# Performance work log

Measured on AMD Instinct MI355X. Metric: run time of the kernel, lower is better.

## Reference

```python
import jax, jax.numpy as jnp
import numpy as np

K = 512       # knowledge_n = node count AND feature dim
S = 50000     # student_n
E_N = 6       # exer_n (hardcoded as literal 6 in the original forward)
DEG_K = 4     # exercise neighbors per knowledge node
DEG_S = 3     # exercise neighbors per student
NEG_SLOPE = 0.2  # PyG GATConv default


def setup_inputs() -> dict:
    key = jax.random.key(0)
    ks = jax.random.split(key, 10)
    kn_emb = jax.random.normal(ks[0], (K, K), jnp.float32)
    exer_emb = jax.random.normal(ks[1], (E_N, K), jnp.float32)
    all_stu_emb = jax.random.normal(ks[2], (S, K), jnp.float32)
    # k_from_e graph: nodes = [exercises(0..5), knowledge(6..6+K-1)]
    src_ke = jax.random.randint(ks[3], (K * DEG_K,), 0, E_N)
    dst_ke = E_N + jnp.repeat(jnp.arange(K), DEG_K)
    edges_ke = jnp.stack([src_ke, dst_ke]).astype(jnp.int32)   # e -> k
    edges_ek = edges_ke[::-1]                                  # k -> e
    # u_from_e graph: nodes = [exercises(0..5), students(6..6+S-1)]
    src_ue = jax.random.randint(ks[4], (S * DEG_S,), 0, E_N)
    dst_ue = E_N + jnp.repeat(jnp.arange(S), DEG_S)
    edges_ue = jnp.stack([src_ue, dst_ue]).astype(jnp.int32)   # e -> u
    edges_eu = edges_ue[::-1]                                  # u -> e
    sc = 1.0 / np.sqrt(K)
    W_gat = jax.random.normal(ks[5], (4, K, K), jnp.float32) * sc
    a_src = jax.random.normal(ks[6], (4, K), jnp.float32) * sc
    a_dst = jax.random.normal(ks[7], (4, K), jnp.float32) * sc
    b_gat = jnp.zeros((4, K), jnp.float32)
    attn_w = jax.random.normal(ks[8], (3, 2 * K), jnp.float32) / np.sqrt(2 * K)
    attn_b = jnp.zeros((3,), jnp.float32)
    return dict(kn_emb=kn_emb, exer_emb=exer_emb, all_stu_emb=all_stu_emb,
                W_gat=W_gat, a_src=a_src, a_dst=a_dst, b_gat=b_gat,
                attn_w=attn_w, attn_b=attn_b,
                edges_ke=edges_ke, edges_ek=edges_ek,
                edges_ue=edges_ue, edges_eu=edges_eu)


def _gat(x, edges, W, a_s, a_d, b, n):
    """Single-head PyG GATConv with self-loops. edges[0]=src, edges[1]=dst."""
    h = x @ W                                   # [n, K]
    loop = jnp.arange(n, dtype=edges.dtype)
    src = jnp.concatenate([edges[0], loop])
    dst = jnp.concatenate([edges[1], loop])
    alpha_s = h @ a_s                           # [n]
    alpha_d = h @ a_d
    e = jax.nn.leaky_relu(alpha_s[src] + alpha_d[dst], NEG_SLOPE)
    emax = jax.lax.stop_gradient(jax.ops.segment_max(e, dst, num_segments=n))
    ex = jnp.exp(e - emax[dst])
    den = jax.ops.segment_sum(ex, dst, num_segments=n)
    alpha = ex / den[dst]                       # per-dst softmax
    out = jax.ops.segment_sum(alpha[:, None] * h[src], dst, num_segments=n)
    return out + b


def reference(kn_emb, exer_emb, all_stu_emb, W_gat, a_src, a_dst, b_gat,
              attn_w, attn_b, edges_ke, edges_ek, edges_ue, edges_eu):
    e_k = jnp.concatenate([exer_emb, kn_emb], axis=0)        # [6+K, K]
    e_u = jnp.concatenate([exer_emb, all_stu_emb], axis=0)   # [6+S, K]
    n_ek, n_eu = e_k.shape[0], e_u.shape[0]
    k_from_e = _gat(e_k, edges_ke, W_gat[0], a_src[0], a_dst[0], b_gat[0], n_ek)
    e_from_k = _gat(e_k, edges_ek, W_gat[1], a_src[1], a_dst[1], b_gat[1], n_ek)
    u_from_e = _gat(e_u, edges_ue, W_gat[2], a_src[2], a_dst[2], b_gat[2], n_eu)
    e_from_u = _gat(e_u, edges_eu, W_gat[3], a_src[3], a_dst[3], b_gat[3], n_eu)
    # knowledge fusion (softmax over a single column -> all ones, kept faithful)
    D = k_from_e[E_N:]
    s3 = jnp.concatenate([kn_emb, D], axis=1) @ attn_w[0] + attn_b[0]   # [K]
    sc = jax.nn.softmax(s3[:, None], axis=1)
    kn_out = kn_emb + sc[:, 0:1] * D
    # exercise fusion: 2-way attention over knowledge/student messages
    B = e_from_k[:E_N]
    C = e_from_u[:E_N]
    s1 = jnp.concatenate([exer_emb, B], axis=1) @ attn_w[1] + attn_b[1]
    s2 = jnp.concatenate([exer_emb, C], axis=1) @ attn_w[2] + attn_b[2]
    sc2 = jax.nn.softmax(jnp.stack([s1, s2], axis=1), axis=1)           # [6, 2]
    exer_out = exer_emb + sc2[:, 0:1] * B + sc2[:, 1:2] * C
    stu_out = all_stu_emb + u_from_e[E_N:]
    return (kn_out, exer_out, stu_out)
```

## Files before the change

kernel.cpp:

```cpp
#include <hip/hip_runtime.h>

typedef __attribute__((ext_vector_type(4))) float f4;
typedef __attribute__((ext_vector_type(8))) short s8;

__device__ __forceinline__ unsigned short f2bf(float x){
  unsigned u = __float_as_uint(x);
  u += 0x7fffu + ((u >> 16) & 1u);
  return (unsigned short)(u >> 16);
}
__device__ __forceinline__ float lrelu(float v){ return v > 0.f ? v : 0.2f * v; }

__device__ __forceinline__ void gload16(const unsigned short* g, unsigned short* l){
  __builtin_amdgcn_global_load_lds((const __attribute__((address_space(1))) unsigned int*)g,
                                   (__attribute__((address_space(3))) unsigned int*)l, 16, 0, 0);
}

__global__ void prep_pq(const float* __restrict__ Wg, const float* __restrict__ a_src,
                        const float* __restrict__ a_dst, float* __restrict__ pq,
                        float* __restrict__ zbase){
  int tid = blockIdx.x * 256 + threadIdx.x;
  for (int i = tid; i < 18444; i += gridDim.x * 256) zbase[i] = 0.f;
  int wid = tid >> 6, lane = tid & 63;
  for (int task = wid; task < 4096; task += gridDim.x * 4){
    int g = task >> 10, isq = (task >> 9) & 1, r = task & 511;
    const float* w = Wg + ((g * 512 + r) << 9);
    const float* a = (isq ? a_dst : a_src) + g * 512;
    float s = 0.f;
    for (int i = lane; i < 512; i += 64) s += w[i] * a[i];
    for (int off = 32; off; off >>= 1) s += __shfl_down(s, off);
    if (lane == 0) pq[task] = s;
  }
}

__global__ void prep_wt(const float* __restrict__ Wg, unsigned short* __restrict__ W2T,
                        unsigned short* __restrict__ W0T){
  __shared__ float tile[32][33];
  const int b = blockIdx.x;
  const int m = b >> 8;
  const int kb = (b & 15) * 32;
  const int nb = ((b >> 4) & 15) * 32;
  const float* W = Wg + (m == 0 ? 2 * 262144 : 0);
  unsigned short* WT = (m == 0) ? W2T : W0T;
  const int tx = threadIdx.x & 31, ty = threadIdx.x >> 5;
  #pragma unroll
  for (int i = 0; i < 32; i += 8) tile[ty + i][tx] = W[(kb + ty + i) * 512 + nb + tx];
  __syncthreads();
  #pragma unroll
  for (int i = 0; i < 32; i += 8) WT[(nb + ty + i) * 512 + kb + tx] = f2bf(tile[tx][ty + i]);
}

__global__ void prep_scal(const float* __restrict__ exer, const float* __restrict__ pq,
                          float* __restrict__ asE, float* __restrict__ adE){
  const int t = threadIdx.x, wid = t >> 6, lane = t & 63;
  for (int task = wid; task < 48; task += 4){
    int gg = task / 12, rem = task % 12, isq = rem / 6, e = rem % 6;
    const float* X = exer + e * 512;
    const float* V = pq + gg * 1024 + isq * 512;
    float s = 0.f;
    for (int i = lane; i < 512; i += 64) s += X[i] * V[i];
    for (int off = 32; off; off >>= 1) s += __shfl_down(s, off);
    if (lane == 0) (isq ? adE : asE)[gg * 6 + e] = s;
  }
}

__global__ void prep_he(const float* __restrict__ exer, const float* __restrict__ Wg,
                        float* __restrict__ HE2, float* __restrict__ HE0){
  const int b = blockIdx.x;
  const int ks = blockIdx.y;
  const int g = (b < 6) ? 0 : 2;
  const int e = b % 6;
  __shared__ float xs[64];
  const int t = threadIdx.x;
  if (t < 64) xs[t] = exer[e * 512 + ks * 64 + t];
  __syncthreads();
  const float* W = Wg + g * 262144 + ks * 64 * 512;
  float acc = 0.f;
  #pragma unroll 4
  for (int kk = 0; kk < 64; kk++) acc += xs[kk] * W[kk * 512 + t];
  atomicAdd(&((g == 0) ? HE0 : HE2)[e * 512 + t], acc);
}

template<int DEG>
__launch_bounds__(256)
__global__ void pass1(const float* __restrict__ x, const float* __restrict__ pq,
                      int gA, int gB,
                      const float* __restrict__ asE, const float* __restrict__ adE,
                      float* __restrict__ alph, const int* __restrict__ idx,
                      float* __restrict__ Craw, float* __restrict__ den, int M)
{
  __shared__ float sC[3072];
  __shared__ float sDen[6];
  const int tid = threadIdx.x, lane = tid & 63, wid = tid >> 6;
  for (int i = tid; i < 3072; i += 256) sC[i] = 0.f;
  if (tid < 6) sDen[tid] = 0.f;

  const int kb = lane * 8;
  const float* pqA = pq + gA * 1024;
  const float* pqB = pq + gB * 1024;
  f4 pA0 = *(const f4*)(pqA + kb),       pA1 = *(const f4*)(pqA + kb + 4);
  f4 qA0 = *(const f4*)(pqA + 512 + kb), qA1 = *(const f4*)(pqA + 512 + kb + 4);
  f4 pB0 = *(const f4*)(pqB + kb),       pB1 = *(const f4*)(pqB + kb + 4);
  float aseR = asE[gA * 6 + (lane % 6)];
  float adeR = adE[gB * 6 + (lane % 6)];

  float cacc[6][8];
  #pragma unroll
  for (int e = 0; e < 6; e++)
    #pragma unroll
    for (int i = 0; i < 8; i++) cacc[e][i] = 0.f;
  float dacc[6] = {0.f,0.f,0.f,0.f,0.f,0.f};
  __syncthreads();

  const int gw = blockIdx.x * 4 + wid, nw = gridDim.x * 4;
  for (int r = gw; r < M; r += nw){
    const float* xr = x + (size_t)r * 512;
    f4 x0 = *(const f4*)(xr + kb), x1 = *(const f4*)(xr + kb + 4);
    float dP = 0.f, dQ = 0.f, dB = 0.f;
    #pragma unroll
    for (int i = 0; i < 4; i++){
      dP += x0[i]*pA0[i] + x1[i]*pA1[i];
      dQ += x0[i]*qA0[i] + x1[i]*qA1[i];
      dB += x0[i]*pB0[i] + x1[i]*pB1[i];
    }
    #pragma unroll
    for (int off = 1; off < 64; off <<= 1){
      dP += __shfl_xor(dP, off); dQ += __shfl_xor(dQ, off); dB += __shfl_xor(dB, off);
    }
    int ei[DEG];
    #pragma unroll
    for (int j = 0; j < DEG; j++) ei[j] = idx[r * DEG + j];
    float scS = lrelu(dP + dQ);
    float sc[DEG], m = scS;
    #pragma unroll
    for (int j = 0; j < DEG; j++){ sc[j] = lrelu(__shfl(aseR, ei[j]) + dQ); m = fmaxf(m, sc[j]); }
    float eS = __expf(scS - m), sum = eS;
    float ev[DEG];
    #pragma unroll
    for (int j = 0; j < DEG; j++){ ev[j] = __expf(sc[j] - m); sum += ev[j]; }
    float inv = 1.f / sum;
    float val = 0.f;
    if (lane == 0) val = eS * inv;
    else if (lane < 7){
      #pragma unroll
      for (int j = 0; j < DEG; j++) val += (ei[j] == lane - 1) ? ev[j] * inv : 0.f;
    }
    if (lane < 8) alph[(size_t)r * 8 + lane] = val;
    float wj[DEG];
    #pragma unroll
    for (int j = 0; j < DEG; j++) wj[j] = __expf(lrelu(dB + __shfl(adeR, ei[j])));
    #pragma unroll
    for (int e = 0; e < 6; e++){
      float we = 0.f;
      #pragma unroll
      for (int j = 0; j < DEG; j++) we += (ei[j] == e) ? wj[j] : 0.f;
      dacc[e] += we;
      #pragma unroll
      for (int i = 0; i < 4; i++){ cacc[e][i] += we * x0[i]; cacc[e][4+i] += we * x1[i]; }
    }
  }
  #pragma unroll
  for (int e = 0; e < 6; e++)
    #pragma unroll
    for (int i = 0; i < 8; i++)
      atomicAdd(&sC[e * 512 + kb + i], cacc[e][i]);
  if (lane == 0){
    #pragma unroll
    for (int e = 0; e < 6; e++) atomicAdd(&sDen[e], dacc[e]);
  }
  __syncthreads();
  for (int i = tid; i < 3072; i += 256){
    float v = sC[i];
    if (v != 0.f) atomicAdd(&Craw[i], v);
  }
  if (tid < 6) atomicAdd(&den[tid], sDen[tid]);
}

__launch_bounds__(512, 4)
__global__ void gemm_ep(const float* __restrict__ x, const unsigned short* __restrict__ WT,
                        const float* __restrict__ alph, const float* __restrict__ HE,
                        const float* __restrict__ bA, float* __restrict__ outp, int M)
{
  __shared__ __align__(16) unsigned short sB[32768];
  __shared__ __align__(16) float sAl[1024];
  __shared__ __align__(16) float sHEb[384];
  __shared__ __align__(16) float sBias[64];

  const int nwg = gridDim.x;
  const int xcd = blockIdx.x & 7, pos = blockIdx.x >> 3;
  const int wido = xcd * (nwg >> 3) + pos;
  const int mb = wido >> 3, nb = wido & 7;
  const int r0 = mb * 128, n0 = nb * 64;
  const int tid = threadIdx.x, lane = tid & 63, w = tid >> 6;
  const int l16 = lane & 15, lhi = lane >> 4;

  {
    const int row = (tid >> 6), slot = tid & 63;
    #pragma unroll
    for (int it = 0; it < 8; it++){
      const int rr = it * 8 + row;
      const unsigned short* src = WT + (size_t)(n0 + rr) * 512 + ((slot ^ (rr & 7)) << 3);
      gload16(src, sB + it * 4096 + tid * 8);
    }
  }
  if (tid < 256){
    const int row = tid >> 1;
    *(f4*)(sAl + tid * 4) = *(const f4*)(alph + (size_t)min(r0 + row, M - 1) * 8 + (tid & 1) * 4);
  } else if (tid < 352){
    const int idx2 = tid - 256, e = idx2 >> 4, c4 = idx2 & 15;
    *(f4*)(sHEb + e * 64 + c4 * 4) = *(const f4*)(HE + e * 512 + n0 + c4 * 4);
  } else if (tid < 368){
    const int idx2 = tid - 352;
    *(f4*)(sBias + idx2 * 4) = *(const f4*)(bA + n0 + idx2 * 4);
  }
  __syncthreads();

  const int gr0 = r0 + w * 16 + l16;
  const float* xr = x + (size_t)min(gr0, M - 1) * 512 + lhi * 8;

  f4 acc[4];
  #pragma unroll
  for (int n = 0; n < 4; n++) acc[n] = (f4){0.f, 0.f, 0.f, 0.f};

  #pragma unroll 4
  for (int kt = 0; kt < 16; kt++){
    f4 a0 = *(const f4*)(xr + kt * 32);
    f4 a1 = *(const f4*)(xr + kt * 32 + 4);
    s8 af;
    #pragma unroll
    for (int i = 0; i < 4; i++){ af[i] = (short)f2bf(a0[i]); af[4+i] = (short)f2bf(a1[i]); }
    #pragma unroll
    for (int n = 0; n < 4; n++){
      const int row = n * 16 + l16;
      const int slot = ((kt << 2) + lhi) ^ (row & 7);
      s8 bf = *(const s8*)(sB + row * 512 + (slot << 3));
      acc[n] = __builtin_amdgcn_mfma_f32_16x16x32_bf16(af, bf, acc[n], 0, 0, 0);
    }
  }

  float hec[4][6], bias[4];
  #pragma unroll
  for (int n = 0; n < 4; n++){
    bias[n] = sBias[n * 16 + l16];
    #pragma unroll
    for (int e = 0; e < 6; e++) hec[n][e] = sHEb[e * 64 + n * 16 + l16];
  }

  #pragma unroll
  for (int j = 0; j < 4; j++){
    const int rl = w * 16 + lhi * 4 + j;
    const int gr = r0 + rl;
    if (gr < M){
      f4 alA = *(const f4*)(sAl + rl * 8);
      f4 alB = *(const f4*)(sAl + rl * 8 + 4);
      const float aself = alA[0];
      #pragma unroll
      for (int n = 0; n < 4; n++){
        const int gc = n0 + n * 16 + l16;
        float v = x[(size_t)gr * 512 + gc] + aself * acc[n][j] + bias[n];
        v += alA[1] * hec[n][0] + alA[2] * hec[n][1] + alA[3] * hec[n][2];
        v += alB[0] * hec[n][3] + alB[1] * hec[n][4] + alB[2] * hec[n][5];
        outp[(size_t)gr * 512 + gc] = v;
      }
    }
  }
}

__global__ void finalize_bc(const float* __restrict__ exer, const float* __restrict__ Wg,
                            const float* __restrict__ asE, const float* __restrict__ adE,
                            const float* __restrict__ Craw3, const float* __restrict__ den3,
                            const float* __restrict__ Craw1, const float* __restrict__ den1,
                            const float* __restrict__ b_gat, float* __restrict__ B,
                            float* __restrict__ C){
  const int b = blockIdx.x;
  const int ks = blockIdx.y;
  const int isC = (b >= 6) ? 1 : 0;
  const int e = b % 6;
  const int g = isC ? 3 : 1;
  const float* Craw = isC ? Craw3 : Craw1;
  const float* den  = isC ? den3  : den1;
  __shared__ float mix[64];
  const int t = threadIdx.x;
  float aS = asE[g*6 + e], aD = adE[g*6 + e];
  float wself = __expf(lrelu(aS + aD));
  float dn = den[e] + wself;
  if (t < 64){
    int k = ks * 64 + t;
    mix[t] = (Craw[e*512 + k] + wself * exer[e*512 + k]) / dn;
  }
  __syncthreads();
  const float* W = Wg + g * 262144 + ks * 64 * 512;
  float acc = 0.f;
  #pragma unroll 4
  for (int kk = 0; kk < 64; kk++) acc += mix[kk] * W[kk * 512 + t];
  if (ks == 0) acc += b_gat[g*512 + t];
  atomicAdd(&(isC ? C : B)[e*512 + t], acc);
}

__global__ void finalize_exer(const float* __restrict__ exer, const float* __restrict__ B,
                              const float* __restrict__ C, const float* __restrict__ attn_w,
                              const float* __restrict__ attn_b, float* __restrict__ outE){
  __shared__ float s1[6], s2[6];
  const int t = threadIdx.x, wid = t >> 6, lane = t & 63;
  for (int task = wid; task < 12; task += 8){
    int e = task >> 1, which = task & 1;
    const float* w = attn_w + (which + 1) * 1024;
    const float* X = exer + e * 512;
    const float* Y = (which ? C : B) + e * 512;
    float s = 0.f;
    for (int i = lane; i < 512; i += 64) s += X[i] * w[i] + Y[i] * w[512 + i];
    for (int off = 32; off; off >>= 1) s += __shfl_down(s, off);
    if (lane == 0) (which ? s2 : s1)[e] = s + attn_b[which + 1];
  }
  __syncthreads();
  for (int i = t; i < 3072; i += 512){
    int e = i >> 9;
    float a = s1[e], b = s2[e];
    float m = fmaxf(a, b);
    float ea = __expf(a - m), eb = __expf(b - m);
    float inv = 1.f / (ea + eb);
    outE[i] = exer[i] + (ea * inv) * B[i] + (eb * inv) * C[i];
  }
}

extern "C" void kernel_launch(void* const* d_in, const int* in_sizes, int n_in,
                              void* d_out, int out_size, void* d_ws, size_t ws_size,
                              hipStream_t stream){
  const float* kn     = (const float*)d_in[0];
  const float* exer   = (const float*)d_in[1];
  const float* stu    = (const float*)d_in[2];
  const float* Wg     = (const float*)d_in[3];
  const float* a_src  = (const float*)d_in[4];
  const float* a_dst  = (const float*)d_in[5];
  const float* b_gat  = (const float*)d_in[6];
  const float* attn_w = (const float*)d_in[7];
  const float* attn_b = (const float*)d_in[8];
  const int*   e_ke   = (const int*)d_in[9];
  const int*   e_ue   = (const int*)d_in[11];
  float* out = (float*)d_out;

  unsigned short* W2T = (unsigned short*)d_ws;
  unsigned short* W0T = W2T + 262144;
  float* fb    = (float*)(W0T + 262144);
  float* pq    = fb;
  float* asE   = pq + 4096;
  float* adE   = asE + 24;
  float* Craw3 = adE + 24;
  float* Craw1 = Craw3 + 3072;
  float* den3  = Craw1 + 3072;
  float* den1  = den3 + 6;
  float* HE2   = den1 + 6;
  float* HE0   = HE2 + 3072;
  float* Bb    = HE0 + 3072;
  float* Cc    = Bb + 3072;
  float* alphS = Cc + 3072;
  float* alphK = alphS + 400384;

  hipLaunchKernelGGL(prep_pq, dim3(256), dim3(256), 0, stream, Wg, a_src, a_dst, pq, Craw3);
  hipLaunchKernelGGL(prep_wt, dim3(512), dim3(256), 0, stream, Wg, W2T, W0T);
  hipLaunchKernelGGL(prep_scal, dim3(1), dim3(256), 0, stream, exer, pq, asE, adE);
  hipLaunchKernelGGL(prep_he, dim3(12, 8), dim3(512), 0, stream, exer, Wg, HE2, HE0);

  hipLaunchKernelGGL((pass1<3>), dim3(768), dim3(256), 0, stream,
                     stu, pq, 2, 3, asE, adE, alphS, e_ue, Craw3, den3, 50000);
  hipLaunchKernelGGL((pass1<4>), dim3(8), dim3(256), 0, stream,
                     kn, pq, 0, 1, asE, adE, alphK, e_ke, Craw1, den1, 512);

  hipLaunchKernelGGL(gemm_ep, dim3(391 * 8), dim3(512), 0, stream,
                     stu, W2T, alphS, HE2, b_gat + 1024, out + 265216, 50000);
  hipLaunchKernelGGL(gemm_ep, dim3(4 * 8), dim3(512), 0, stream,
                     kn, W0T, alphK, HE0, b_gat, out, 512);

  hipLaunchKernelGGL(finalize_bc, dim3(12, 8), dim3(512), 0, stream,
                     exer, Wg, asE, adE, Craw3, den3, Craw1, den1, b_gat, Bb, Cc);
  hipLaunchKernelGGL(finalize_exer, dim3(1), dim3(512), 0, stream,
                     exer, Bb, Cc, attn_w, attn_b, out + 262144);
}
```

Measured before the change: 485.2 us.

## Fuse attention pass and GEMM epilogue into one kernel with LDS-staged activations

Result: slower. 656.4 us (+35.3%).

```diff
diff --git a/kernel.cpp b/kernel.cpp
--- a/kernel.cpp
+++ b/kernel.cpp
@@ -9,11 +9,6 @@
   return (unsigned short)(u >> 16);
 }
 __device__ __forceinline__ float lrelu(float v){ return v > 0.f ? v : 0.2f * v; }
-
-__device__ __forceinline__ void gload16(const unsigned short* g, unsigned short* l){
-  __builtin_amdgcn_global_load_lds((const __attribute__((address_space(1))) unsigned int*)g,
-                                   (__attribute__((address_space(3))) unsigned int*)l, 16, 0, 0);
-}
 
 __global__ void prep_pq(const float* __restrict__ Wg, const float* __restrict__ a_src,
                         const float* __restrict__ a_dst, float* __restrict__ pq,
@@ -81,186 +76,159 @@
 }
 
 template<int DEG>
-__launch_bounds__(256)
-__global__ void pass1(const float* __restrict__ x, const float* __restrict__ pq,
-                      int gA, int gB,
-                      const float* __restrict__ asE, const float* __restrict__ adE,
-                      float* __restrict__ alph, const int* __restrict__ idx,
-                      float* __restrict__ Craw, float* __restrict__ den, int M)
+__launch_bounds__(512, 4)
+__global__ void fused(const float* __restrict__ x, const unsigned short* __restrict__ WT,
+                      const float* __restrict__ pqA, const float* __restrict__ pqB,
+                      const float* __restrict__ asEg, const float* __restrict__ adEg,
+                      const float* __restrict__ HE, const float* __restrict__ bias,
+                      const int* __restrict__ idx, float* __restrict__ Craw,
+                      float* __restrict__ den, float* __restrict__ outp, int M)
 {
-  __shared__ float sC[3072];
-  __shared__ float sDen[6];
-  const int tid = threadIdx.x, lane = tid & 63, wid = tid >> 6;
-  for (int i = tid; i < 3072; i += 256) sC[i] = 0.f;
-  if (tid < 6) sDen[tid] = 0.f;
-
-  const int kb = lane * 8;
-  const float* pqA = pq + gA * 1024;
-  const float* pqB = pq + gB * 1024;
-  f4 pA0 = *(const f4*)(pqA + kb),       pA1 = *(const f4*)(pqA + kb + 4);
-  f4 qA0 = *(const f4*)(pqA + 512 + kb), qA1 = *(const f4*)(pqA + 512 + kb + 4);
-  f4 pB0 = *(const f4*)(pqB + kb),       pB1 = *(const f4*)(pqB + kb + 4);
-  float aseR = asE[gA * 6 + (lane % 6)];
-  float adeR = adE[gB * 6 + (lane % 6)];
-
-  float cacc[6][8];
-  #pragma unroll
-  for (int e = 0; e < 6; e++)
-    #pragma unroll
-    for (int i = 0; i < 8; i++) cacc[e][i] = 0.f;
-  float dacc[6] = {0.f,0.f,0.f,0.f,0.f,0.f};
-  __syncthreads();
-
-  const int gw = blockIdx.x * 4 + wid, nw = gridDim.x * 4;
-  for (int r = gw; r < M; r += nw){
-    const float* xr = x + (size_t)r * 512;
-    f4 x0 = *(const f4*)(xr + kb), x1 = *(const f4*)(xr + kb + 4);
+  __shared__ __align__(16) unsigned short sA[32768];
+  __shared__ float sMeta[64][16];
+  __shared__ float sDot[3][64];
+
+  const int tid = threadIdx.x, lane = tid & 63, w = tid >> 6;
+  const int r0 = blockIdx.x * 64;
+  const int kseg = (lane ^ w) * 8;
+
+  f4 pP0 = *(const f4*)(pqA + kseg),       pP1 = *(const f4*)(pqA + kseg + 4);
+  f4 pQ0 = *(const f4*)(pqA + 512 + kseg), pQ1 = *(const f4*)(pqA + 512 + kseg + 4);
+  f4 pB0 = *(const f4*)(pqB + kseg),       pB1 = *(const f4*)(pqB + kseg + 4);
+
+  #pragma unroll
+  for (int i = 0; i < 8; i++){
+    const int row = i * 8 + w;
+    const float* xr = x + (size_t)min(r0 + row, M - 1) * 512 + kseg;
+    f4 x0 = *(const f4*)(xr), x1 = *(const f4*)(xr + 4);
     float dP = 0.f, dQ = 0.f, dB = 0.f;
     #pragma unroll
-    for (int i = 0; i < 4; i++){
-      dP += x0[i]*pA0[i] + x1[i]*pA1[i];
-      dQ += x0[i]*qA0[i] + x1[i]*qA1[i];
-      dB += x0[i]*pB0[i] + x1[i]*pB1[i];
+    for (int c = 0; c < 4; c++){
+      dP += x0[c]*pP0[c] + x1[c]*pP1[c];
+      dQ += x0[c]*pQ0[c] + x1[c]*pQ1[c];
+      dB += x0[c]*pB0[c] + x1[c]*pB1[c];
     }
     #pragma unroll
     for (int off = 1; off < 64; off <<= 1){
       dP += __shfl_xor(dP, off); dQ += __shfl_xor(dQ, off); dB += __shfl_xor(dB, off);
     }
+    if (lane == 0){ sDot[0][row] = dP; sDot[1][row] = dQ; sDot[2][row] = dB; }
+    s8 pk;
+    #pragma unroll
+    for (int c = 0; c < 4; c++){ pk[c] = (short)f2bf(x0[c]); pk[4+c] = (short)f2bf(x1[c]); }
+    *(s8*)(sA + row * 512 + lane * 8) = pk;
+  }
+  __syncthreads();
+
+  if (w == 0){
+    const int r = lane, gr = r0 + r;
+    const bool valid = gr < M;
+    const float dP = sDot[0][r], dQ = sDot[1][r], dB = sDot[2][r];
     int ei[DEG];
     #pragma unroll
-    for (int j = 0; j < DEG; j++) ei[j] = idx[r * DEG + j];
+    for (int j = 0; j < DEG; j++) ei[j] = valid ? idx[(size_t)gr * DEG + j] : 0;
     float scS = lrelu(dP + dQ);
     float sc[DEG], m = scS;
     #pragma unroll
-    for (int j = 0; j < DEG; j++){ sc[j] = lrelu(__shfl(aseR, ei[j]) + dQ); m = fmaxf(m, sc[j]); }
+    for (int j = 0; j < DEG; j++){ sc[j] = lrelu(asEg[ei[j]] + dQ); m = fmaxf(m, sc[j]); }
     float eS = __expf(scS - m), sum = eS;
     float ev[DEG];
     #pragma unroll
     for (int j = 0; j < DEG; j++){ ev[j] = __expf(sc[j] - m); sum += ev[j]; }
-    float inv = 1.f / sum;
-    float val = 0.f;
-    if (lane == 0) val = eS * inv;
-    else if (lane < 7){
-      #pragma unroll
-      for (int j = 0; j < DEG; j++) val += (ei[j] == lane - 1) ? ev[j] * inv : 0.f;
-    }
-    if (lane < 8) alph[(size_t)r * 8 + lane] = val;
+    const float inv = 1.f / sum;
+    sMeta[r][0] = valid ? eS * inv : 0.f;
     float wj[DEG];
     #pragma unroll
-    for (int j = 0; j < DEG; j++) wj[j] = __expf(lrelu(dB + __shfl(adeR, ei[j])));
+    for (int j = 0; j < DEG; j++) wj[j] = __expf(lrelu(dB + adEg[ei[j]]));
     #pragma unroll
     for (int e = 0; e < 6; e++){
-      float we = 0.f;
-      #pragma unroll
-      for (int j = 0; j < DEG; j++) we += (ei[j] == e) ? wj[j] : 0.f;
-      dacc[e] += we;
-      #pragma unroll
-      for (int i = 0; i < 4; i++){ cacc[e][i] += we * x0[i]; cacc[e][4+i] += we * x1[i]; }
-    }
-  }
-  #pragma unroll
-  for (int e = 0; e < 6; e++)
-    #pragma unroll
-    for (int i = 0; i < 8; i++)
-      atomicAdd(&sC[e * 512 + kb + i], cacc[e][i]);
-  if (lane == 0){
-    #pragma unroll
-    for (int e = 0; e < 6; e++) atomicAdd(&sDen[e], dacc[e]);
-  }
-  __syncthreads();
-  for (int i = tid; i < 3072; i += 256){
-    float v = sC[i];
-    if (v != 0.f) atomicAdd(&Craw[i], v);
-  }
-  if (tid < 6) atomicAdd(&den[tid], sDen[tid]);
-}
-
-__launch_bounds__(512, 4)
-__global__ void gemm_ep(const float* __restrict__ x, const unsigned short* __restrict__ WT,
-                        const float* __restrict__ alph, const float* __restrict__ HE,
-                        const float* __restrict__ bA, float* __restrict__ outp, int M)
-{
-  __shared__ __align__(16) unsigned short sB[32768];
-  __shared__ __align__(16) float sAl[1024];
-  __shared__ __align__(16) float sHEb[384];
-  __shared__ __align__(16) float sBias[64];
-
-  const int nwg = gridDim.x;
-  const int xcd = blockIdx.x & 7, pos = blockIdx.x >> 3;
-  const int wido = xcd * (nwg >> 3) + pos;
-  const int mb = wido >> 3, nb = wido & 7;
-  const int r0 = mb * 128, n0 = nb * 64;
-  const int tid = threadIdx.x, lane = tid & 63, w = tid >> 6;
+      float ce = 0.f, we = 0.f;
+      #pragma unroll
+      for (int j = 0; j < DEG; j++){
+        ce += (ei[j] == e) ? ev[j] * inv : 0.f;
+        we += (ei[j] == e) ? wj[j] : 0.f;
+      }
+      sMeta[r][1 + e] = valid ? ce : 0.f;
+      we = valid ? we : 0.f;
+      sMeta[r][7 + e] = we;
+      float t = we;
+      #pragma unroll
+      for (int off = 1; off < 64; off <<= 1) t += __shfl_xor(t, off);
+      if (lane == 0) atomicAdd(den + e, t);
+    }
+  }
+
   const int l16 = lane & 15, lhi = lane >> 4;
-
-  {
-    const int row = (tid >> 6), slot = tid & 63;
-    #pragma unroll
-    for (int it = 0; it < 8; it++){
-      const int rr = it * 8 + row;
-      const unsigned short* src = WT + (size_t)(n0 + rr) * 512 + ((slot ^ (rr & 7)) << 3);
-      gload16(src, sB + it * 4096 + tid * 8);
-    }
-  }
-  if (tid < 256){
-    const int row = tid >> 1;
-    *(f4*)(sAl + tid * 4) = *(const f4*)(alph + (size_t)min(r0 + row, M - 1) * 8 + (tid & 1) * 4);
-  } else if (tid < 352){
-    const int idx2 = tid - 256, e = idx2 >> 4, c4 = idx2 & 15;
-    *(f4*)(sHEb + e * 64 + c4 * 4) = *(const f4*)(HE + e * 512 + n0 + c4 * 4);
-  } else if (tid < 368){
-    const int idx2 = tid - 352;
-    *(f4*)(sBias + idx2 * 4) = *(const f4*)(bA + n0 + idx2 * 4);
-  }
-  __syncthreads();
-
-  const int gr0 = r0 + w * 16 + l16;
-  const float* xr = x + (size_t)min(gr0, M - 1) * 512 + lhi * 8;
-
-  f4 acc[4];
-  #pragma unroll
-  for (int n = 0; n < 4; n++) acc[n] = (f4){0.f, 0.f, 0.f, 0.f};
+  const unsigned short* wtb = WT + (size_t)(w * 64 + l16) * 512 + lhi * 8;
+  f4 acc[4][4];
+  #pragma unroll
+  for (int m = 0; m < 4; m++)
+    #pragma unroll
+    for (int n = 0; n < 4; n++) acc[m][n] = (f4){0.f, 0.f, 0.f, 0.f};
 
   #pragma unroll 4
   for (int kt = 0; kt < 16; kt++){
-    f4 a0 = *(const f4*)(xr + kt * 32);
-    f4 a1 = *(const f4*)(xr + kt * 32 + 4);
-    s8 af;
-    #pragma unroll
-    for (int i = 0; i < 4; i++){ af[i] = (short)f2bf(a0[i]); af[4+i] = (short)f2bf(a1[i]); }
+    s8 af[4];
+    #pragma unroll
+    for (int m = 0; m < 4; m++)
+      af[m] = *(const s8*)(sA + (m * 16 + l16) * 512 + ((((kt << 2) | lhi)) ^ (l16 & 7)) * 8);
     #pragma unroll
     for (int n = 0; n < 4; n++){
-      const int row = n * 16 + l16;
-      const int slot = ((kt << 2) + lhi) ^ (row & 7);
-      s8 bf = *(const s8*)(sB + row * 512 + (slot << 3));
-      acc[n] = __builtin_amdgcn_mfma_f32_16x16x32_bf16(af, bf, acc[n], 0, 0, 0);
-    }
-  }
-
-  float hec[4][6], bias[4];
+      s8 bf = *(const s8*)(wtb + (size_t)n * 16 * 512 + kt * 32);
+      #pragma unroll
+      for (int m = 0; m < 4; m++)
+        acc[m][n] = __builtin_amdgcn_mfma_f32_16x16x32_bf16(af[m], bf, acc[m][n], 0, 0, 0);
+    }
+  }
+  __syncthreads();
+
+  float hec[4][6], bi[4];
   #pragma unroll
   for (int n = 0; n < 4; n++){
-    bias[n] = sBias[n * 16 + l16];
-    #pragma unroll
-    for (int e = 0; e < 6; e++) hec[n][e] = sHEb[e * 64 + n * 16 + l16];
-  }
-
-  #pragma unroll
-  for (int j = 0; j < 4; j++){
-    const int rl = w * 16 + lhi * 4 + j;
-    const int gr = r0 + rl;
-    if (gr < M){
-      f4 alA = *(const f4*)(sAl + rl * 8);
-      f4 alB = *(const f4*)(sAl + rl * 8 + 4);
-      const float aself = alA[0];
+    const int gc = w * 64 + n * 16 + l16;
+    bi[n] = bias[gc];
+    #pragma unroll
+    for (int e = 0; e < 6; e++) hec[n][e] = HE[e * 512 + gc];
+  }
+  float creg[4][6];
+  #pragma unroll
+  for (int n = 0; n < 4; n++)
+    #pragma unroll
+    for (int e = 0; e < 6; e++) creg[n][e] = 0.f;
+
+  #pragma unroll
+  for (int m = 0; m < 4; m++){
+    #pragma unroll
+    for (int j = 0; j < 4; j++){
+      const int rl = m * 16 + lhi * 4 + j;
+      const int gr = r0 + rl;
+      const bool v = gr < M;
+      const float aself = sMeta[rl][0];
+      float wrow[6], crow[6];
+      #pragma unroll
+      for (int e = 0; e < 6; e++){ wrow[e] = sMeta[rl][7 + e]; crow[e] = sMeta[rl][1 + e]; }
       #pragma unroll
       for (int n = 0; n < 4; n++){
-        const int gc = n0 + n * 16 + l16;
-        float v = x[(size_t)gr * 512 + gc] + aself * acc[n][j] + bias[n];
-        v += alA[1] * hec[n][0] + alA[2] * hec[n][1] + alA[3] * hec[n][2];
-        v += alB[0] * hec[n][3] + alB[1] * hec[n][4] + alB[2] * hec[n][5];
-        outp[(size_t)gr * 512 + gc] = v;
+        const int gc = w * 64 + n * 16 + l16;
+        const float xv = v ? x[(size_t)gr * 512 + gc] : 0.f;
+        if (v){
+          float o = xv + aself * acc[m][n][j] + bi[n];
+          #pragma unroll
+          for (int e = 0; e < 6; e++) o += crow[e] * hec[n][e];
+          outp[(size_t)gr * 512 + gc] = o;
+        }
+        #pragma unroll
+        for (int e = 0; e < 6; e++) creg[n][e] += wrow[e] * xv;
       }
+    }
+  }
+  #pragma unroll
+  for (int n = 0; n < 4; n++){
+    #pragma unroll
+    for (int e = 0; e < 6; e++){
+      float vv = creg[n][e];
+      vv += __shfl_xor(vv, 16); vv += __shfl_xor(vv, 32);
+      if (lhi == 0) atomicAdd(&Craw[e * 512 + w * 64 + n * 16 + l16], vv);
     }
   }
 }
@@ -352,23 +320,18 @@
   float* HE0   = HE2 + 3072;
   float* Bb    = HE0 + 3072;
   float* Cc    = Bb + 3072;
-  float* alphS = Cc + 3072;
-  float* alphK = alphS + 400384;
 
   hipLaunchKernelGGL(prep_pq, dim3(256), dim3(256), 0, stream, Wg, a_src, a_dst, pq, Craw3);
   hipLaunchKernelGGL(prep_wt, dim3(512), dim3(256), 0, stream, Wg, W2T, W0T);
   hipLaunchKernelGGL(prep_scal, dim3(1), dim3(256), 0, stream, exer, pq, asE, adE);
   hipLaunchKernelGGL(prep_he, dim3(12, 8), dim3(512), 0, stream, exer, Wg, HE2, HE0);
 
-  hipLaunchKernelGGL((pass1<3>), dim3(768), dim3(256), 0, stream,
-                     stu, pq, 2, 3, asE, adE, alphS, e_ue, Craw3, den3, 50000);
-  hipLaunchKernelGGL((pass1<4>), dim3(8), dim3(256), 0, stream,
-                     kn, pq, 0, 1, asE, adE, alphK, e_ke, Craw1, den1, 512);
-
-  hipLaunchKernelGGL(gemm_ep, dim3(391 * 8), dim3(512), 0, stream,
-                     stu, W2T, alphS, HE2, b_gat + 1024, out + 265216, 50000);
-  hipLaunchKernelGGL(gemm_ep, dim3(4 * 8), dim3(512), 0, stream,
-                     kn, W0T, alphK, HE0, b_gat, out, 512);
+  hipLaunchKernelGGL((fused<3>), dim3(782), dim3(512), 0, stream,
+                     stu, W2T, pq + 2048, pq + 3072, asE + 12, adE + 18,
+                     HE2, b_gat + 1024, e_ue, Craw3, den3, out + 265216, 50000);
+  hipLaunchKernelGGL((fused<4>), dim3(8), dim3(512), 0, stream,
+                     kn, W0T, pq, pq + 1024, asE, adE + 6,
+                     HE0, b_gat, e_ke, Craw1, den1, out, 512);
 
   hipLaunchKernelGGL(finalize_bc, dim3(12, 8), dim3(512), 0, stream,
                      exer, Wg, asE, adE, Craw3, den3, Craw1, den1, b_gat, Bb, Cc);
```
